# Optimization experiments

Measured on AMD Instinct MI355X. Metric: run time of the kernel, lower is better.

The kernel has to match this reference:

```python
import jax, jax.numpy as jnp
import numpy as np


def setup_inputs() -> dict:
    key = jax.random.key(0)
    k1, k2, k3, k4 = jax.random.split(key, 4)
    b, c_in, t, h, w = 8, 64, 16, 64, 64
    c_out, kh, kw = 64, 3, 3
    x = jax.random.normal(k1, (b, c_in, t, h, w), dtype=jnp.float32)
    alpha = jax.random.uniform(k2, (b, c_in, t, 1, 1), dtype=jnp.float32)
    fan_in = c_in * kh * kw
    weight = jax.random.normal(k3, (c_out, c_in, kh, kw), dtype=jnp.float32) / np.sqrt(fan_in)
    bias = jax.random.normal(k4, (c_out,), dtype=jnp.float32) * 0.05
    return {"x": x, "alpha": alpha, "weight": weight, "bias": bias}


def reference(x, alpha, weight, bias):
    # x: (b, c_in, t, h, w); alpha: (b, c_in, t, 1, 1)
    # weight: (c_out, c_in, kh, kw); bias: (c_out,)
    b, c_in, t, h, w = x.shape
    c_out, _, kh, kw = weight.shape
    pad = ((kh // 2, kh // 2), (kw // 2, kw // 2))  # padding=1 for 3x3
    # per-(b,t) calibrated weights: alpha scales the c_in dim (cal_dim='cin')
    a = jnp.transpose(alpha[..., 0, 0], (0, 2, 1))          # (b, t, c_in)
    w_bt = a[:, :, None, :, None, None] * weight[None, None]  # (b, t, c_out, c_in, kh, kw)
    xs = jnp.transpose(x, (0, 2, 1, 3, 4)).reshape(b * t, 1, c_in, h, w)
    ws = w_bt.reshape(b * t, c_out, c_in, kh, kw)

    def conv_one(xi, wi):
        return jax.lax.conv_general_dilated(
            xi, wi, window_strides=(1, 1), padding=pad,
            dimension_numbers=("NCHW", "OIHW", "NCHW"))[0]

    out = jax.vmap(conv_one)(xs, ws)                          # (b*t, c_out, h, w)
    out = out + bias[None, :, None, None]
    out = out.reshape(b, t, c_out, h, w).transpose(0, 2, 1, 3, 4)
    return out  # (b, c_out, t, h, w)
```

## Files before the change

kernel.cpp:

```cpp
#include <hip/hip_runtime.h>


#define CIN  64
#define COUT 64
#define TT   16
#define BB   8
#define HH   64
#define WW   64

typedef __attribute__((ext_vector_type(8))) short bf16x8;
typedef __attribute__((ext_vector_type(4))) float f32x4;

__device__ __forceinline__ unsigned short f2bf(float f) {
    union { float f; unsigned u; } v; v.f = f;
    unsigned r = (v.u + 0x7FFF + ((v.u >> 16) & 1)) >> 16;
    return (unsigned short)r;
}

__global__ __launch_bounds__(256) void prep_w(const float* __restrict__ wgt,
                                              unsigned short* __restrict__ wb) {
    int idx = blockIdx.x * 256 + threadIdx.x;
    if (idx < COUT * CIN * 9) {
        int co  = idx / (CIN * 9);
        int r   = idx - co * (CIN * 9);
        int ci  = r / 9;
        int tap = r - ci * 9;
        int q    = co >> 4;
        int co_l = co & 15;
        int kc   = ci >> 5;
        int kg   = (ci >> 3) & 3;
        int e    = ci & 7;
        wb[(((((q * 9 + tap) * 2 + kc) * 4 + kg) * 16) + co_l) * 8 + e] = f2bf(wgt[idx]);
    }
}

__global__ __launch_bounds__(512, 4) void conv4(const float* __restrict__ x,
                                                const float* __restrict__ alpha,
                                                const short* __restrict__ wb,
                                                const float* __restrict__ bias,
                                                float* __restrict__ out) {
    __shared__ __align__(16) short xs[6 * 66 * 64];

    const int orig  = blockIdx.x;
    const int blk   = (orig & 7) * 256 + (orig >> 3);
    const int ytile = blk & 15;
    const int bt    = blk >> 4;
    const int t     = bt & 15;
    const int b     = bt >> 4;
    const int y0    = ytile * 4;
    const int tid   = threadIdx.x;
    const int wv    = tid >> 6;
    const int lane  = tid & 63;
    const int co_l  = lane & 15;
    const int kg    = lane >> 4;
    const int q     = wv & 3;
    const int ph    = wv >> 2;

    bf16x8 wreg[9][2];
#pragma unroll
    for (int tap = 0; tap < 9; ++tap)
#pragma unroll
        for (int kc = 0; kc < 2; ++kc)
            wreg[tap][kc] = *(const bf16x8*)(wb + (((q * 9 + tap) * 2 + kc) * 64 + lane) * 8);

    {
        const int cib = wv * 8;
        float a0 = alpha[(b * CIN + cib + 0) * TT + t];
        float a1 = alpha[(b * CIN + cib + 1) * TT + t];
        float a2 = alpha[(b * CIN + cib + 2) * TT + t];
        float a3 = alpha[(b * CIN + cib + 3) * TT + t];
        float a4 = alpha[(b * CIN + cib + 4) * TT + t];
        float a5 = alpha[(b * CIN + cib + 5) * TT + t];
        float a6 = alpha[(b * CIN + cib + 6) * TT + t];
        float a7 = alpha[(b * CIN + cib + 7) * TT + t];
        const float* xb = x + (size_t)((b * CIN + cib) * TT + t) * (HH * WW);
        const int slot = wv ^ (lane & 7);
        const int CI_STRIDE = TT * HH * WW;
#pragma unroll
        for (int r = 0; r < 6; ++r) {
            const int gy = y0 - 1 + r;
            int4 o = {0, 0, 0, 0};
            if ((unsigned)gy < HH) {
                const float* p = xb + gy * WW + lane;
                float v0 = p[0 * CI_STRIDE] * a0;
                float v1 = p[1 * CI_STRIDE] * a1;
                float v2 = p[2 * CI_STRIDE] * a2;
                float v3 = p[3 * CI_STRIDE] * a3;
                float v4 = p[4 * CI_STRIDE] * a4;
                float v5 = p[5 * CI_STRIDE] * a5;
                float v6 = p[6 * CI_STRIDE] * a6;
                float v7 = p[7 * CI_STRIDE] * a7;
                o.x = (int)f2bf(v0) | ((int)f2bf(v1) << 16);
                o.y = (int)f2bf(v2) | ((int)f2bf(v3) << 16);
                o.z = (int)f2bf(v4) | ((int)f2bf(v5) << 16);
                o.w = (int)f2bf(v6) | ((int)f2bf(v7) << 16);
            }
            *(int4*)(xs + r * 4224 + (lane + 1) * 64 + slot * 8) = o;
            if (lane < 2) {
                int4 z = {0, 0, 0, 0};
                *(int4*)(xs + r * 4224 + lane * 65 * 64 + wv * 8) = z;
            }
        }
    }
    __syncthreads();

    f32x4 acc[2][4] = {};
    int si[3][2];
#pragma unroll
    for (int dxi = 0; dxi < 3; ++dxi)
#pragma unroll
        for (int kc = 0; kc < 2; ++kc) {
            int wx = co_l + dxi - 1;
            si[dxi][kc] = (wx + 1) * 64 + (((kc * 4 + kg) ^ (wx & 7)) * 8);
        }

#pragma unroll
    for (int tap = 0; tap < 9; ++tap) {
        const int ky  = tap / 3;
        const int dxi = tap - 3 * ky;
        const int rb  = (ph * 2 + ky) * 4224;
#pragma unroll
        for (int kc = 0; kc < 2; ++kc) {
#pragma unroll
            for (int r = 0; r < 2; ++r) {
                const short* rowp = xs + rb + r * 4224 + si[dxi][kc];
#pragma unroll
                for (int n = 0; n < 4; ++n) {
                    bf16x8 bfr = *(const bf16x8*)(rowp + n * 1024);
                    acc[r][n] = __builtin_amdgcn_mfma_f32_16x16x32_bf16(
                        wreg[tap][kc], bfr, acc[r][n], 0, 0, 0);
                }
            }
        }
    }

#pragma unroll
    for (int r = 0; r < 2; ++r) {
        const int y = y0 + ph * 2 + r;
#pragma unroll
        for (int rr = 0; rr < 4; ++rr) {
            const int co = q * 16 + kg * 4 + rr;
            const float bv = bias[co];
            float* op = out + (size_t)(((b * COUT + co) * TT + t) * HH + y) * WW;
#pragma unroll
            for (int n = 0; n < 4; ++n)
                op[n * 16 + co_l] = acc[r][n][rr] + bv;
        }
    }
}

extern "C" void kernel_launch(void* const* d_in, const int* in_sizes, int n_in,
                              void* d_out, int out_size, void* d_ws, size_t ws_size,
                              hipStream_t stream) {
    const float* x      = (const float*)d_in[0];
    const float* alpha  = (const float*)d_in[1];
    const float* weight = (const float*)d_in[2];
    const float* bias   = (const float*)d_in[3];
    float* out          = (float*)d_out;

    unsigned short* wb = (unsigned short*)d_ws;

    hipLaunchKernelGGL(prep_w, dim3(144), dim3(256), 0, stream, weight, wb);
    hipLaunchKernelGGL(conv4, dim3(BB * TT * (HH / 4)), dim3(512), 0, stream,
                       x, alpha, (const short*)wb, bias, out);
}
```

Baseline: 269.7 us.

## Shrink conv tile to two output rows with waves sharing B fragments across two cout groups

Each block now covers 2 output rows with 256 threads instead of 4 rows with 512. Each wave holds weights for two 16-channel output groups and reuses every LDS B fragment for two MFMAs, which halves LDS reads per MFMA. The cost is a larger halo: each block loads 4 input rows for 2 output rows instead of 6 for 4, so more redundant global reads and bf16 conversion. Weight registers double and launch bounds drop to 2 blocks of 256, which lowers occupancy.

```diff
diff --git a/kernel.cpp b/kernel.cpp
--- a/kernel.cpp
+++ b/kernel.cpp
@@ -34,71 +34,69 @@
     }
 }
 
-__global__ __launch_bounds__(512, 4) void conv4(const float* __restrict__ x,
+__global__ __launch_bounds__(256, 2) void conv5(const float* __restrict__ x,
                                                 const float* __restrict__ alpha,
                                                 const short* __restrict__ wb,
                                                 const float* __restrict__ bias,
                                                 float* __restrict__ out) {
-    __shared__ __align__(16) short xs[6 * 66 * 64];
+    __shared__ __align__(16) short xs[4 * 4224];
 
     const int orig  = blockIdx.x;
-    const int blk   = (orig & 7) * 256 + (orig >> 3);
-    const int ytile = blk & 15;
-    const int bt    = blk >> 4;
+    const int blk   = (orig & 7) * 512 + (orig >> 3);
+    const int ytile = blk & 31;
+    const int bt    = blk >> 5;
     const int t     = bt & 15;
     const int b     = bt >> 4;
-    const int y0    = ytile * 4;
+    const int y0    = ytile * 2;
     const int tid   = threadIdx.x;
     const int wv    = tid >> 6;
     const int lane  = tid & 63;
     const int co_l  = lane & 15;
     const int kg    = lane >> 4;
-    const int q     = wv & 3;
-    const int ph    = wv >> 2;
+    const int mg    = wv >> 1;
+    const int rw    = wv & 1;
 
-    bf16x8 wreg[9][2];
+    bf16x8 wreg[2][9][2];
 #pragma unroll
-    for (int tap = 0; tap < 9; ++tap)
+    for (int m = 0; m < 2; ++m)
 #pragma unroll
-        for (int kc = 0; kc < 2; ++kc)
-            wreg[tap][kc] = *(const bf16x8*)(wb + (((q * 9 + tap) * 2 + kc) * 64 + lane) * 8);
+        for (int tap = 0; tap < 9; ++tap)
+#pragma unroll
+            for (int kc = 0; kc < 2; ++kc)
+                wreg[m][tap][kc] = *(const bf16x8*)(
+                    wb + ((((mg * 2 + m) * 9 + tap) * 2 + kc) * 64 + lane) * 8);
 
     {
-        const int cib = wv * 8;
-        float a0 = alpha[(b * CIN + cib + 0) * TT + t];
-        float a1 = alpha[(b * CIN + cib + 1) * TT + t];
-        float a2 = alpha[(b * CIN + cib + 2) * TT + t];
-        float a3 = alpha[(b * CIN + cib + 3) * TT + t];
-        float a4 = alpha[(b * CIN + cib + 4) * TT + t];
-        float a5 = alpha[(b * CIN + cib + 5) * TT + t];
-        float a6 = alpha[(b * CIN + cib + 6) * TT + t];
-        float a7 = alpha[(b * CIN + cib + 7) * TT + t];
-        const float* xb = x + (size_t)((b * CIN + cib) * TT + t) * (HH * WW);
-        const int slot = wv ^ (lane & 7);
-        const int CI_STRIDE = TT * HH * WW;
+        const int ci0 = wv * 16;
+        if (lane < 16) {
+            int4 z = {0, 0, 0, 0};
+            *(int4*)(xs + wv * 4224 + (lane >> 3) * 4160 + (lane & 7) * 8) = z;
+        }
 #pragma unroll
-        for (int r = 0; r < 6; ++r) {
+        for (int r = 0; r < 4; ++r) {
             const int gy = y0 - 1 + r;
-            int4 o = {0, 0, 0, 0};
-            if ((unsigned)gy < HH) {
-                const float* p = xb + gy * WW + lane;
-                float v0 = p[0 * CI_STRIDE] * a0;
-                float v1 = p[1 * CI_STRIDE] * a1;
-                float v2 = p[2 * CI_STRIDE] * a2;
-                float v3 = p[3 * CI_STRIDE] * a3;
-                float v4 = p[4 * CI_STRIDE] * a4;
-                float v5 = p[5 * CI_STRIDE] * a5;
-                float v6 = p[6 * CI_STRIDE] * a6;
-                float v7 = p[7 * CI_STRIDE] * a7;
-                o.x = (int)f2bf(v0) | ((int)f2bf(v1) << 16);
-                o.y = (int)f2bf(v2) | ((int)f2bf(v3) << 16);
-                o.z = (int)f2bf(v4) | ((int)f2bf(v5) << 16);
-                o.w = (int)f2bf(v6) | ((int)f2bf(v7) << 16);
-            }
-            *(int4*)(xs + r * 4224 + (lane + 1) * 64 + slot * 8) = o;
-            if (lane < 2) {
-                int4 z = {0, 0, 0, 0};
-                *(int4*)(xs + r * 4224 + lane * 65 * 64 + wv * 8) = z;
+            short* rowb = xs + r * 4224;
+#pragma unroll
+            for (int gi = 0; gi < 2; ++gi) {
+                const int g  = wv * 2 + gi;
+                const int cg = ci0 + gi * 8;
+                int4 o = {0, 0, 0, 0};
+                if ((unsigned)gy < HH) {
+                    const float* p = x + ((size_t)((b * CIN + cg) * TT + t) * HH + gy) * WW + lane;
+                    float v0 = p[0 * 65536] * alpha[(b * CIN + cg + 0) * TT + t];
+                    float v1 = p[1 * 65536] * alpha[(b * CIN + cg + 1) * TT + t];
+                    float v2 = p[2 * 65536] * alpha[(b * CIN + cg + 2) * TT + t];
+                    float v3 = p[3 * 65536] * alpha[(b * CIN + cg + 3) * TT + t];
+                    float v4 = p[4 * 65536] * alpha[(b * CIN + cg + 4) * TT + t];
+                    float v5 = p[5 * 65536] * alpha[(b * CIN + cg + 5) * TT + t];
+                    float v6 = p[6 * 65536] * alpha[(b * CIN + cg + 6) * TT + t];
+                    float v7 = p[7 * 65536] * alpha[(b * CIN + cg + 7) * TT + t];
+                    o.x = (int)f2bf(v0) | ((int)f2bf(v1) << 16);
+                    o.y = (int)f2bf(v2) | ((int)f2bf(v3) << 16);
+                    o.z = (int)f2bf(v4) | ((int)f2bf(v5) << 16);
+                    o.w = (int)f2bf(v6) | ((int)f2bf(v7) << 16);
+                }
+                *(int4*)(rowb + (lane + 1) * 64 + ((g ^ (lane & 7)) * 8)) = o;
             }
         }
     }
@@ -118,33 +116,32 @@
     for (int tap = 0; tap < 9; ++tap) {
         const int ky  = tap / 3;
         const int dxi = tap - 3 * ky;
-        const int rb  = (ph * 2 + ky) * 4224;
+        const short* rowp = xs + (rw + ky) * 4224;
 #pragma unroll
         for (int kc = 0; kc < 2; ++kc) {
+            const short* bp = rowp + si[dxi][kc];
 #pragma unroll
-            for (int r = 0; r < 2; ++r) {
-                const short* rowp = xs + rb + r * 4224 + si[dxi][kc];
-#pragma unroll
-                for (int n = 0; n < 4; ++n) {
-                    bf16x8 bfr = *(const bf16x8*)(rowp + n * 1024);
-                    acc[r][n] = __builtin_amdgcn_mfma_f32_16x16x32_bf16(
-                        wreg[tap][kc], bfr, acc[r][n], 0, 0, 0);
-                }
+            for (int n = 0; n < 4; ++n) {
+                bf16x8 bfr = *(const bf16x8*)(bp + n * 1024);
+                acc[0][n] = __builtin_amdgcn_mfma_f32_16x16x32_bf16(
+                    wreg[0][tap][kc], bfr, acc[0][n], 0, 0, 0);
+                acc[1][n] = __builtin_amdgcn_mfma_f32_16x16x32_bf16(
+                    wreg[1][tap][kc], bfr, acc[1][n], 0, 0, 0);
             }
         }
     }
 
+    const int y = y0 + rw;
 #pragma unroll
-    for (int r = 0; r < 2; ++r) {
-        const int y = y0 + ph * 2 + r;
+    for (int m = 0; m < 2; ++m) {
 #pragma unroll
         for (int rr = 0; rr < 4; ++rr) {
-            const int co = q * 16 + kg * 4 + rr;
+            const int co = (mg * 2 + m) * 16 + kg * 4 + rr;
             const float bv = bias[co];
             float* op = out + (size_t)(((b * COUT + co) * TT + t) * HH + y) * WW;
 #pragma unroll
             for (int n = 0; n < 4; ++n)
-                op[n * 16 + co_l] = acc[r][n][rr] + bv;
+                op[n * 16 + co_l] = acc[m][n][rr] + bv;
         }
     }
 }
@@ -161,6 +158,6 @@
     unsigned short* wb = (unsigned short*)d_ws;
 
     hipLaunchKernelGGL(prep_w, dim3(144), dim3(256), 0, stream, weight, wb);
-    hipLaunchKernelGGL(conv4, dim3(BB * TT * (HH / 4)), dim3(512), 0, stream,
+    hipLaunchKernelGGL(conv5, dim3(BB * TT * (HH / 2)), dim3(256), 0, stream,
                        x, alpha, (const short*)wb, bias, out);
 }
```

Result: slower. 278.0 us (+3.1%).
